# Kernel optimization log

Hardware: AMD Instinct MI355X
Metric: run time of the kernel (lower is better)

Reference implementation:

```python
import jax, jax.numpy as jnp
import numpy as np

H = 128          # hidden_size
IN = 93          # input_size
NL = 4           # num_layers
B, T = 256, 512  # batch, seq_len


def setup_inputs() -> dict:
    key = jax.random.key(0)
    ks = jax.random.split(key, 8)
    s = 1.0 / np.sqrt(H)  # pytorch LSTM init range scale
    x = jax.random.normal(ks[0], (B, T, IN), jnp.float32)
    W_ih0 = jax.random.normal(ks[1], (4 * H, IN), jnp.float32) * s   # layer 0 input weights
    W_ih_rest = jax.random.normal(ks[2], (NL - 1, 4 * H, H), jnp.float32) * s  # layers 1..3
    W_hh = jax.random.normal(ks[3], (NL, 4 * H, H), jnp.float32) * s
    b_ih = jax.random.normal(ks[4], (NL, 4 * H), jnp.float32) * s
    b_hh = jax.random.normal(ks[5], (NL, 4 * H), jnp.float32) * s
    W_fc = jax.random.normal(ks[6], (1, H), jnp.float32) * s
    b_fc = jax.random.normal(ks[7], (1,), jnp.float32) * s
    return {"x": x, "W_ih0": W_ih0, "W_ih_rest": W_ih_rest, "W_hh": W_hh,
            "b_ih": b_ih, "b_hh": b_hh, "W_fc": W_fc, "b_fc": b_fc}


def _lstm_layer(x_tm, W_ih, W_hh_l, bi, bh):
    # x_tm: [T, B, in]; precompute input-side gates as one big GEMM
    gates_x = jnp.einsum('tbi,gi->tbg', x_tm, W_ih) + bi + bh  # [T,B,4H]

    def step(carry, gx):
        h, c = carry
        g = gx + h @ W_hh_l.T                      # [B,4H]
        i, f, gg, o = jnp.split(g, 4, axis=-1)     # pytorch gate order: i,f,g,o
        i = jax.nn.sigmoid(i)
        f = jax.nn.sigmoid(f)
        gg = jnp.tanh(gg)
        o = jax.nn.sigmoid(o)
        c = f * c + i * gg
        h = o * jnp.tanh(c)
        return (h, c), h

    b = x_tm.shape[1]
    h0 = jnp.zeros((b, H), x_tm.dtype)
    (_, _), hs = jax.lax.scan(step, (h0, h0), gates_x)
    return hs  # [T,B,H]


def reference(x, W_ih0, W_ih_rest, W_hh, b_ih, b_hh, W_fc, b_fc):
    # Eval-mode forward (dropout inactive), matching model.eval() semantics.
    h = jnp.transpose(x, (1, 0, 2))  # time-major [T,B,IN]
    h = _lstm_layer(h, W_ih0, W_hh[0], b_ih[0], b_hh[0])
    for l in range(1, NL):
        h = _lstm_layer(h, W_ih_rest[l - 1], W_hh[l], b_ih[l], b_hh[l])
    out = jax.nn.sigmoid(jnp.einsum('tbh,oh->tbo', h, W_fc) + b_fc)  # [T,B,1]
    return jnp.transpose(out, (1, 0, 2))  # [B,T,1]
```

## Files before the change

### kernel.cpp

```cpp
#include <hip/hip_runtime.h>
#include <hip/hip_bf16.h>

#define H_    128
#define IN_   93
#define NL_   4
#define B_    256
#define T_    512
#define G_    512
#define C_    32
#define NCH   (T_ / C_)
#define NLAUNCH (NCH + NL_ - 1)
#define LOG2E 1.44269504088896f
#define BH_   (B_ * H_)
#define B96_  (B_ * 96)

typedef __attribute__((ext_vector_type(8))) short bf16x8;
typedef __attribute__((ext_vector_type(4))) float f32x4;
typedef unsigned long long u64;

#define RCHUNK ((size_t)C_ * BH_)

__device__ __forceinline__ ushort bf16_rn(float f) {
    uint x = __float_as_uint(f);
    uint r = (x + 0x7FFFu + ((x >> 16) & 1u)) >> 16;
    return (ushort)r;
}
__device__ __forceinline__ float exp2_fast(float x) { return __builtin_amdgcn_exp2f(x); }
__device__ __forceinline__ float rcp_fast(float x)  { return __builtin_amdgcn_rcpf(x); }

__global__ void prep_x(const float* __restrict__ x, ushort* __restrict__ xb) {
    int idx = blockIdx.x * 256 + threadIdx.x;
    int t = idx / (B_ * 96);
    int rem = idx % (B_ * 96);
    int b = rem / 96;
    int k = rem % 96;
    float v = 0.0f;
    if (k < IN_) v = x[((size_t)b * T_ + t) * IN_ + k];
    xb[idx] = bf16_rn(v);
}

__global__ void prep_w(const float* __restrict__ Wih0,
                       const float* __restrict__ Wihr,
                       const float* __restrict__ Whh,
                       ushort* __restrict__ Wc) {
    int idx = blockIdx.x * 256 + threadIdx.x;
    int l = idx / (G_ * 256);
    int rem = idx % (G_ * 256);
    int g = rem / 256;
    int k = rem % 256;
    int kx = (l == 0) ? 96 : 128;
    float v = 0.0f;
    if (k < kx) {
        if (l == 0) { if (k < IN_) v = Wih0[g * IN_ + k]; }
        else        { v = Wihr[(((size_t)(l - 1)) * G_ + g) * H_ + k]; }
    } else if (k < kx + H_) {
        v = Whh[(((size_t)l) * G_ + g) * H_ + (k - kx)];
    }
    float scale = (g >= 256 && g < 384) ? (2.0f * LOG2E) : LOG2E;
    Wc[idx] = bf16_rn(v * scale);
}

__global__ void prep_bias(const float* __restrict__ bih,
                          const float* __restrict__ bhh,
                          float* __restrict__ bc) {
    int idx = blockIdx.x * 256 + threadIdx.x;
    int g = idx & 511;
    float scale = (g >= 256 && g < 384) ? (2.0f * LOG2E) : LOG2E;
    bc[idx] = (bih[idx] + bhh[idx]) * scale;
}

#define SWZC(row, col) ((col) ^ (((row) & 7) << 3))
#define XRD(ts, s) (*(const bf16x8*)&hist[(ts) * 2048 + lo * 128 + \
                     ((((s) << 5) | (q << 3)) ^ ((lo & 7) << 3))])
#define HRD(ptr, s) (*(const bf16x8*)&(ptr)[lo * 128 + \
                     ((((s) << 5) | (q << 3)) ^ ((lo & 7) << 3))])
#define MF(a, av, bw) a = __builtin_amdgcn_mfma_f32_16x16x32_bf16(av, bw, a, 0, 0, 0)

__global__ __launch_bounds__(512, 2)
void recur_chunk(const ushort* __restrict__ xb,
                 const ushort* __restrict__ Wc,
                 const float* __restrict__ biasc,
                 ushort* __restrict__ ring,
                 ushort* __restrict__ seed3,
                 float*  __restrict__ cstate,
                 const float* __restrict__ wfc,
                 const float* __restrict__ bfc,
                 float* __restrict__ out,
                 int wlaunch) {
    __shared__ ushort hist[C_ * 16 * 128];
    __shared__ ushort seedb[16 * 128];
    __shared__ float  wfs[H_];

    const int bid = blockIdx.x;
    const int l = bid >> 4;
    const int g = bid & 15;
    const int k = wlaunch - l;
    if (k < 0 || k >= NCH) return;

    const bool lz = (l == 0);
    const int t0 = k * C_;

    const int tid = threadIdx.x;
    const int wv  = tid >> 6;
    const int ln  = tid & 63;
    const int q   = ln >> 4;
    const int lo  = ln & 15;
    const int u   = (wv << 4) | lo;
    const int b0  = g << 4;

    const ushort* Wl = Wc + (size_t)l * G_ * 256;
    const float*  bl = biasc + l * G_;
    const int kx = lz ? 96 : 128;

    ushort* ring_self = ring + (size_t)(2 * l + (k & 1)) * RCHUNK;
    const ushort* ring_up = ring + (size_t)(2 * (l - 1) + (k & 1)) * RCHUNK;

    if (tid < H_) wfs[tid] = wfc[tid];

    for (int i = tid; i < C_ * 16 * 32; i += 512) {
        int t = i >> 9, rem = i & 511, row = rem >> 5, c8 = rem & 31;
        u64 v = 0;
        if (lz) {
            if (c8 < 24)
                v = *(const u64*)(xb + (size_t)(t0 + t) * B96_ +
                                  (size_t)(b0 + row) * 96 + (c8 << 2));
        } else {
            v = *(const u64*)(ring_up + (size_t)t * BH_ +
                              (size_t)(b0 + row) * H_ + (c8 << 2));
        }
        *(u64*)&hist[t * 2048 + row * 128 + SWZC(row, c8 << 2)] = v;
    }

    {
        int row = tid >> 5, c8 = tid & 31;
        u64 v = 0;
        if (k > 0) {
            if (l < 3) {
                v = *(const u64*)(ring + (size_t)(2 * l + ((k - 1) & 1)) * RCHUNK +
                                  (size_t)(C_ - 1) * BH_ +
                                  (size_t)(b0 + row) * H_ + (c8 << 2));
            } else {
                v = *(const u64*)(seed3 + (size_t)(b0 + row) * H_ + (c8 << 2));
            }
        }
        *(u64*)&seedb[row * 128 + SWZC(row, c8 << 2)] = v;
    }

    bf16x8 bwx[4][4], bwh[4][4];
#pragma unroll
    for (int tu = 0; tu < 4; ++tu)
#pragma unroll
        for (int s = 0; s < 4; ++s) {
            const ushort* rowp = Wl + ((size_t)((tu << 7) + u) << 8);
            bwx[tu][s] = *(const bf16x8*)(rowp + (s << 5) + (q << 3));
            bwh[tu][s] = *(const bf16x8*)(rowp + kx + (s << 5) + (q << 3));
        }

    const float bv0 = bl[u];
    const float bv1 = bl[128 + u];
    const float bv2 = bl[256 + u];
    const float bv3 = bl[384 + u];

    f32x4 cc = {0.0f, 0.0f, 0.0f, 0.0f};
    if (k > 0) {
#pragma unroll
        for (int r = 0; r < 4; ++r)
            cc[r] = cstate[(((size_t)(l * 16 + g)) * 16 + (q << 2) + r) * 128 + u];
    }

    __syncthreads();

    f32x4 ac0 = {bv0, bv0, bv0, bv0};
    f32x4 ac1 = {bv1, bv1, bv1, bv1};
    f32x4 ac2 = {bv2, bv2, bv2, bv2};
    f32x4 ac3 = {bv3, bv3, bv3, bv3};
    {
        bf16x8 x0 = XRD(0, 0), x1 = XRD(0, 1), x2 = XRD(0, 2), x3 = XRD(0, 3);
        MF(ac0, x0, bwx[0][0]); MF(ac1, x0, bwx[1][0]); MF(ac2, x0, bwx[2][0]); MF(ac3, x0, bwx[3][0]);
        MF(ac0, x1, bwx[0][1]); MF(ac1, x1, bwx[1][1]); MF(ac2, x1, bwx[2][1]); MF(ac3, x1, bwx[3][1]);
        MF(ac0, x2, bwx[0][2]); MF(ac1, x2, bwx[1][2]); MF(ac2, x2, bwx[2][2]); MF(ac3, x2, bwx[3][2]);
        MF(ac0, x3, bwx[0][3]); MF(ac1, x3, bwx[1][3]); MF(ac2, x3, bwx[2][3]); MF(ac3, x3, bwx[3][3]);
    }

    for (int t = 0; t < C_; ++t) {
        asm volatile("s_waitcnt lgkmcnt(0)" ::: "memory");
        __builtin_amdgcn_s_barrier();
        __builtin_amdgcn_sched_barrier(0);

        const ushort* hsrc = (t == 0) ? seedb : &hist[(t - 1) * 2048];
        bf16x8 h0 = HRD(hsrc, 0), h1 = HRD(hsrc, 1), h2 = HRD(hsrc, 2), h3v = HRD(hsrc, 3);
        MF(ac0, h0, bwh[0][0]); MF(ac1, h0, bwh[1][0]); MF(ac2, h0, bwh[2][0]); MF(ac3, h0, bwh[3][0]);
        MF(ac0, h1, bwh[0][1]); MF(ac1, h1, bwh[1][1]); MF(ac2, h1, bwh[2][1]); MF(ac3, h1, bwh[3][1]);
        MF(ac0, h2, bwh[0][2]); MF(ac1, h2, bwh[1][2]); MF(ac2, h2, bwh[2][2]); MF(ac3, h2, bwh[3][2]);
        MF(ac0, h3v, bwh[0][3]); MF(ac1, h3v, bwh[1][3]); MF(ac2, h3v, bwh[2][3]); MF(ac3, h3v, bwh[3][3]);

        f32x4 an0 = {bv0, bv0, bv0, bv0};
        f32x4 an1 = {bv1, bv1, bv1, bv1};
        f32x4 an2 = {bv2, bv2, bv2, bv2};
        f32x4 an3 = {bv3, bv3, bv3, bv3};
        if (t + 1 < C_) {
            bf16x8 x0 = XRD(t + 1, 0), x1 = XRD(t + 1, 1), x2 = XRD(t + 1, 2), x3 = XRD(t + 1, 3);
            MF(an0, x0, bwx[0][0]); MF(an1, x0, bwx[1][0]); MF(an2, x0, bwx[2][0]); MF(an3, x0, bwx[3][0]);
            MF(an0, x1, bwx[0][1]); MF(an1, x1, bwx[1][1]); MF(an2, x1, bwx[2][1]); MF(an3, x1, bwx[3][1]);
            MF(an0, x2, bwx[0][2]); MF(an1, x2, bwx[1][2]); MF(an2, x2, bwx[2][2]); MF(an3, x2, bwx[3][2]);
            MF(an0, x3, bwx[0][3]); MF(an1, x3, bwx[1][3]); MF(an2, x3, bwx[2][3]); MF(an3, x3, bwx[3][3]);
        }

#pragma unroll
        for (int r = 0; r < 4; ++r) {
            float ei = exp2_fast(fminf(-ac0[r], 60.0f));
            float ef = exp2_fast(-ac1[r]);
            float eg = exp2_fast(fminf(-ac2[r], 60.0f));
            float eo = exp2_fast(fminf(-ac3[r], 60.0f));
            float rf  = rcp_fast(1.0f + ef);
            float rig = rcp_fast((1.0f + ei) * (1.0f + eg));
            float cn  = __builtin_fmaf(cc[r], rf, (1.0f - eg) * rig);
            cc[r] = cn;
            float ec  = exp2_fast(fminf(-2.88539008177793f * cn, 60.0f));
            float roc = rcp_fast((1.0f + eo) * (1.0f + ec));
            float h_  = (1.0f - ec) * roc;
            int row = (q << 2) + r;
            hist[t * 2048 + row * 128 + SWZC(row, u)] = bf16_rn(h_);
        }

        ac0 = an0; ac1 = an1; ac2 = an2; ac3 = an3;
    }

    asm volatile("s_waitcnt lgkmcnt(0)" ::: "memory");
    __builtin_amdgcn_s_barrier();
    __builtin_amdgcn_sched_barrier(0);

    if (l < 3) {
        for (int i = tid; i < C_ * 16 * 32; i += 512) {
            int t = i >> 9, rem = i & 511, row = rem >> 5, c8 = rem & 31;
            u64 v = *(const u64*)&hist[t * 2048 + row * 128 + SWZC(row, c8 << 2)];
            *(u64*)(ring_self + (size_t)t * BH_ +
                    (size_t)(b0 + row) * H_ + (c8 << 2)) = v;
        }
    } else {
        int t = tid >> 4, row = tid & 15;
        float acc = 0.0f;
#pragma unroll 8
        for (int c8 = 0; c8 < 32; ++c8) {
            u64 v = *(const u64*)&hist[t * 2048 + row * 128 + SWZC(row, c8 << 2)];
#pragma unroll
            for (int j = 0; j < 4; ++j) {
                float hvf = __uint_as_float(((uint)(ushort)(v >> (16 * j))) << 16);
                acc = __builtin_fmaf(hvf, wfs[(c8 << 2) + j], acc);
            }
        }
        float z = acc + bfc[0];
        out[(size_t)(b0 + row) * T_ + (t0 + t)] =
            rcp_fast(1.0f + exp2_fast(-z * LOG2E));
        int row2 = tid >> 5, c82 = tid & 31;
        u64 v2 = *(const u64*)&hist[(C_ - 1) * 2048 + row2 * 128 + SWZC(row2, c82 << 2)];
        *(u64*)(seed3 + (size_t)(b0 + row2) * H_ + (c82 << 2)) = v2;
    }

#pragma unroll
    for (int r = 0; r < 4; ++r)
        cstate[(((size_t)(l * 16 + g)) * 16 + (q << 2) + r) * 128 + u] = cc[r];
}

extern "C" void kernel_launch(void* const* d_in, const int* in_sizes, int n_in,
                              void* d_out, int out_size, void* d_ws, size_t ws_size,
                              hipStream_t stream) {
    const float* x    = (const float*)d_in[0];
    const float* Wih0 = (const float*)d_in[1];
    const float* Wihr = (const float*)d_in[2];
    const float* Whh  = (const float*)d_in[3];
    const float* bih  = (const float*)d_in[4];
    const float* bhh  = (const float*)d_in[5];
    const float* Wfc  = (const float*)d_in[6];
    const float* bfc  = (const float*)d_in[7];
    float* out = (float*)d_out;

    char* ws = (char*)d_ws;
    const size_t xb_bytes    = (size_t)T_ * B_ * 96 * 2;
    const size_t wc_bytes    = (size_t)NL_ * G_ * 256 * 2;
    const size_t bias_bytes  = (size_t)NL_ * G_ * 4;
    const size_t ring_bytes  = (size_t)6 * RCHUNK * 2;
    const size_t seed3_bytes = (size_t)B_ * H_ * 2;

    ushort* xb    = (ushort*)ws;
    ushort* Wc    = (ushort*)(ws + xb_bytes);
    float*  biasc = (float*)(ws + xb_bytes + wc_bytes);
    ushort* ring  = (ushort*)(ws + xb_bytes + wc_bytes + bias_bytes);
    ushort* seed3 = (ushort*)(ws + xb_bytes + wc_bytes + bias_bytes + ring_bytes);
    float*  cstate= (float*)(ws + xb_bytes + wc_bytes + bias_bytes + ring_bytes + seed3_bytes);

    prep_x<<<(T_ * B_ * 96) / 256, 256, 0, stream>>>(x, xb);
    prep_w<<<(NL_ * G_ * 256) / 256, 256, 0, stream>>>(Wih0, Wihr, Whh, Wc);
    prep_bias<<<(NL_ * G_) / 256, 256, 0, stream>>>(bih, bhh, biasc);

    for (int w = 0; w < NLAUNCH; ++w) {
        recur_chunk<<<NL_ * 16, 512, 0, stream>>>(xb, Wc, biasc, ring, seed3,
                                                  cstate, Wfc, bfc, out, w);
    }
}
```

Measured before the change: 998.7 us.

## Replace per-wavefront kernel launches with a persistent kernel using flag-based layer pipelining

The 19 sequential wavefront launches become a single persistent kernel in which each layer/batch-group block loops over all time chunks. Blocks wait on their upstream layer through global progress and consumer flags spun on with acquire loads, and the double-buffered ring is guarded by consumer acknowledgements. This keeps weights in registers and the cell state on chip across chunks, removing launch gaps and the cstate and seed reloads. It also widens the LDS swizzle to 16 rows and drops some fminf clamps. The cost is the risk of deadlock if the 64 blocks are not all co-resident, plus spin-polling overhead.

```diff
diff --git a/kernel.cpp b/kernel.cpp
--- a/kernel.cpp
+++ b/kernel.cpp
@@ -9,7 +9,6 @@
 #define G_    512
 #define C_    32
 #define NCH   (T_ / C_)
-#define NLAUNCH (NCH + NL_ - 1)
 #define LOG2E 1.44269504088896f
 #define BH_   (B_ * H_)
 #define B96_  (B_ * 96)
@@ -27,6 +26,14 @@
 }
 __device__ __forceinline__ float exp2_fast(float x) { return __builtin_amdgcn_exp2f(x); }
 __device__ __forceinline__ float rcp_fast(float x)  { return __builtin_amdgcn_rcpf(x); }
+
+__device__ __forceinline__ void spin_acq(int* p, int target) {
+    int v = __hip_atomic_load(p, __ATOMIC_ACQUIRE, __HIP_MEMORY_SCOPE_AGENT);
+    while (v < target) {
+        __builtin_amdgcn_s_sleep(2);
+        v = __hip_atomic_load(p, __ATOMIC_ACQUIRE, __HIP_MEMORY_SCOPE_AGENT);
+    }
+}
 
 __global__ void prep_x(const float* __restrict__ x, ushort* __restrict__ xb) {
     int idx = blockIdx.x * 256 + threadIdx.x;
@@ -69,24 +76,26 @@
     bc[idx] = (bih[idx] + bhh[idx]) * scale;
 }
 
-#define SWZC(row, col) ((col) ^ (((row) & 7) << 3))
+__global__ void zero_flags(int* __restrict__ fl) {
+    if (threadIdx.x < 128) fl[threadIdx.x] = 0;
+}
+
+#define SWZ16(row, col) ((col) ^ (((row) & 15) << 3))
 #define XRD(ts, s) (*(const bf16x8*)&hist[(ts) * 2048 + lo * 128 + \
-                     ((((s) << 5) | (q << 3)) ^ ((lo & 7) << 3))])
+                     ((((s) << 5) | (q << 3)) ^ (lo << 3))])
 #define HRD(ptr, s) (*(const bf16x8*)&(ptr)[lo * 128 + \
-                     ((((s) << 5) | (q << 3)) ^ ((lo & 7) << 3))])
+                     ((((s) << 5) | (q << 3)) ^ (lo << 3))])
 #define MF(a, av, bw) a = __builtin_amdgcn_mfma_f32_16x16x32_bf16(av, bw, a, 0, 0, 0)
 
-__global__ __launch_bounds__(512, 2)
-void recur_chunk(const ushort* __restrict__ xb,
-                 const ushort* __restrict__ Wc,
-                 const float* __restrict__ biasc,
-                 ushort* __restrict__ ring,
-                 ushort* __restrict__ seed3,
-                 float*  __restrict__ cstate,
-                 const float* __restrict__ wfc,
-                 const float* __restrict__ bfc,
-                 float* __restrict__ out,
-                 int wlaunch) {
+__global__ __launch_bounds__(512, 1)
+void recur_persist(const ushort* __restrict__ xb,
+                   const ushort* __restrict__ Wc,
+                   const float* __restrict__ biasc,
+                   ushort* __restrict__ ring,
+                   int*    __restrict__ flags,
+                   const float* __restrict__ wfc,
+                   const float* __restrict__ bfc,
+                   float* __restrict__ out) {
     __shared__ ushort hist[C_ * 16 * 128];
     __shared__ ushort seedb[16 * 128];
     __shared__ float  wfs[H_];
@@ -94,11 +103,7 @@
     const int bid = blockIdx.x;
     const int l = bid >> 4;
     const int g = bid & 15;
-    const int k = wlaunch - l;
-    if (k < 0 || k >= NCH) return;
-
     const bool lz = (l == 0);
-    const int t0 = k * C_;
 
     const int tid = threadIdx.x;
     const int wv  = tid >> 6;
@@ -112,39 +117,16 @@
     const float*  bl = biasc + l * G_;
     const int kx = lz ? 96 : 128;
 
-    ushort* ring_self = ring + (size_t)(2 * l + (k & 1)) * RCHUNK;
-    const ushort* ring_up = ring + (size_t)(2 * (l - 1) + (k & 1)) * RCHUNK;
+    int* prog = flags;
+    int* cons = flags + 64;
+    int* pself = prog + (l * 16 + g);
+    int* pup   = prog + ((l - 1) * 16 + g);
+    int* cself = cons + (l * 16 + g);
+    int* cdown = cons + ((l + 1) * 16 + g);
 
     if (tid < H_) wfs[tid] = wfc[tid];
-
-    for (int i = tid; i < C_ * 16 * 32; i += 512) {
-        int t = i >> 9, rem = i & 511, row = rem >> 5, c8 = rem & 31;
-        u64 v = 0;
-        if (lz) {
-            if (c8 < 24)
-                v = *(const u64*)(xb + (size_t)(t0 + t) * B96_ +
-                                  (size_t)(b0 + row) * 96 + (c8 << 2));
-        } else {
-            v = *(const u64*)(ring_up + (size_t)t * BH_ +
-                              (size_t)(b0 + row) * H_ + (c8 << 2));
-        }
-        *(u64*)&hist[t * 2048 + row * 128 + SWZC(row, c8 << 2)] = v;
-    }
-
-    {
-        int row = tid >> 5, c8 = tid & 31;
-        u64 v = 0;
-        if (k > 0) {
-            if (l < 3) {
-                v = *(const u64*)(ring + (size_t)(2 * l + ((k - 1) & 1)) * RCHUNK +
-                                  (size_t)(C_ - 1) * BH_ +
-                                  (size_t)(b0 + row) * H_ + (c8 << 2));
-            } else {
-                v = *(const u64*)(seed3 + (size_t)(b0 + row) * H_ + (c8 << 2));
-            }
-        }
-        *(u64*)&seedb[row * 128 + SWZC(row, c8 << 2)] = v;
-    }
+    ((u64*)seedb)[tid] = 0ull;
+    const float bfc0 = bfc[0];
 
     bf16x8 bwx[4][4], bwh[4][4];
 #pragma unroll
@@ -155,111 +137,132 @@
             bwx[tu][s] = *(const bf16x8*)(rowp + (s << 5) + (q << 3));
             bwh[tu][s] = *(const bf16x8*)(rowp + kx + (s << 5) + (q << 3));
         }
-
     const float bv0 = bl[u];
     const float bv1 = bl[128 + u];
     const float bv2 = bl[256 + u];
     const float bv3 = bl[384 + u];
 
     f32x4 cc = {0.0f, 0.0f, 0.0f, 0.0f};
-    if (k > 0) {
+
+    for (int k = 0; k < NCH; ++k) {
+        const int t0 = k * C_;
+        ushort* ring_self = ring + (size_t)(2 * l + (k & 1)) * RCHUNK;
+        const ushort* ring_up = ring + (size_t)(2 * (l - 1) + (k & 1)) * RCHUNK;
+
+        if (l > 0) spin_acq(pup, k + 1);
+
+        for (int i = tid; i < C_ * 16 * 32; i += 512) {
+            int t = i >> 9, rem = i & 511, row = rem >> 5, c8 = rem & 31;
+            u64 v = 0;
+            if (lz) {
+                if (c8 < 24)
+                    v = *(const u64*)(xb + (size_t)(t0 + t) * B96_ +
+                                      (size_t)(b0 + row) * 96 + (c8 << 2));
+            } else {
+                v = *(const u64*)(ring_up + (size_t)t * BH_ +
+                                  (size_t)(b0 + row) * H_ + (c8 << 2));
+            }
+            *(u64*)&hist[t * 2048 + row * 128 + SWZ16(row, c8 << 2)] = v;
+        }
+        __syncthreads();
+        if (tid == 0 && l > 0)
+            __hip_atomic_store(cself, k + 1, __ATOMIC_RELAXED, __HIP_MEMORY_SCOPE_AGENT);
+
+        f32x4 ac0 = {bv0, bv0, bv0, bv0};
+        f32x4 ac1 = {bv1, bv1, bv1, bv1};
+        f32x4 ac2 = {bv2, bv2, bv2, bv2};
+        f32x4 ac3 = {bv3, bv3, bv3, bv3};
+        {
+            bf16x8 x0 = XRD(0, 0), x1 = XRD(0, 1), x2 = XRD(0, 2), x3 = XRD(0, 3);
+            MF(ac0, x0, bwx[0][0]); MF(ac1, x0, bwx[1][0]); MF(ac2, x0, bwx[2][0]); MF(ac3, x0, bwx[3][0]);
+            MF(ac0, x1, bwx[0][1]); MF(ac1, x1, bwx[1][1]); MF(ac2, x1, bwx[2][1]); MF(ac3, x1, bwx[3][1]);
+            MF(ac0, x2, bwx[0][2]); MF(ac1, x2, bwx[1][2]); MF(ac2, x2, bwx[2][2]); MF(ac3, x2, bwx[3][2]);
+            MF(ac0, x3, bwx[0][3]); MF(ac1, x3, bwx[1][3]); MF(ac2, x3, bwx[2][3]); MF(ac3, x3, bwx[3][3]);
+        }
+
+        for (int t = 0; t < C_; ++t) {
+            asm volatile("s_waitcnt lgkmcnt(0)" ::: "memory");
+            __builtin_amdgcn_s_barrier();
+            __builtin_amdgcn_sched_barrier(0);
+
+            const ushort* hsrc = (t == 0) ? seedb : &hist[(t - 1) * 2048];
+            bf16x8 h0 = HRD(hsrc, 0), h1 = HRD(hsrc, 1), h2 = HRD(hsrc, 2), h3v = HRD(hsrc, 3);
+            MF(ac0, h0, bwh[0][0]); MF(ac1, h0, bwh[1][0]); MF(ac2, h0, bwh[2][0]); MF(ac3, h0, bwh[3][0]);
+            MF(ac0, h1, bwh[0][1]); MF(ac1, h1, bwh[1][1]); MF(ac2, h1, bwh[2][1]); MF(ac3, h1, bwh[3][1]);
+            MF(ac0, h2, bwh[0][2]); MF(ac1, h2, bwh[1][2]); MF(ac2, h2, bwh[2][2]); MF(ac3, h2, bwh[3][2]);
+            MF(ac0, h3v, bwh[0][3]); MF(ac1, h3v, bwh[1][3]); MF(ac2, h3v, bwh[2][3]); MF(ac3, h3v, bwh[3][3]);
+
+            f32x4 an0 = {bv0, bv0, bv0, bv0};
+            f32x4 an1 = {bv1, bv1, bv1, bv1};
+            f32x4 an2 = {bv2, bv2, bv2, bv2};
+            f32x4 an3 = {bv3, bv3, bv3, bv3};
+            if (t + 1 < C_) {
+                bf16x8 x0 = XRD(t + 1, 0), x1 = XRD(t + 1, 1), x2 = XRD(t + 1, 2), x3 = XRD(t + 1, 3);
+                MF(an0, x0, bwx[0][0]); MF(an1, x0, bwx[1][0]); MF(an2, x0, bwx[2][0]); MF(an3, x0, bwx[3][0]);
+                MF(an0, x1, bwx[0][1]); MF(an1, x1, bwx[1][1]); MF(an2, x1, bwx[2][1]); MF(an3, x1, bwx[3][1]);
+                MF(an0, x2, bwx[0][2]); MF(an1, x2, bwx[1][2]); MF(an2, x2, bwx[2][2]); MF(an3, x2, bwx[3][2]);
+                MF(an0, x3, bwx[0][3]); MF(an1, x3, bwx[1][3]); MF(an2, x3, bwx[2][3]); MF(an3, x3, bwx[3][3]);
+            }
+
 #pragma unroll
-        for (int r = 0; r < 4; ++r)
-            cc[r] = cstate[(((size_t)(l * 16 + g)) * 16 + (q << 2) + r) * 128 + u];
-    }
-
-    __syncthreads();
-
-    f32x4 ac0 = {bv0, bv0, bv0, bv0};
-    f32x4 ac1 = {bv1, bv1, bv1, bv1};
-    f32x4 ac2 = {bv2, bv2, bv2, bv2};
-    f32x4 ac3 = {bv3, bv3, bv3, bv3};
-    {
-        bf16x8 x0 = XRD(0, 0), x1 = XRD(0, 1), x2 = XRD(0, 2), x3 = XRD(0, 3);
-        MF(ac0, x0, bwx[0][0]); MF(ac1, x0, bwx[1][0]); MF(ac2, x0, bwx[2][0]); MF(ac3, x0, bwx[3][0]);
-        MF(ac0, x1, bwx[0][1]); MF(ac1, x1, bwx[1][1]); MF(ac2, x1, bwx[2][1]); MF(ac3, x1, bwx[3][1]);
-        MF(ac0, x2, bwx[0][2]); MF(ac1, x2, bwx[1][2]); MF(ac2, x2, bwx[2][2]); MF(ac3, x2, bwx[3][2]);
-        MF(ac0, x3, bwx[0][3]); MF(ac1, x3, bwx[1][3]); MF(ac2, x3, bwx[2][3]); MF(ac3, x3, bwx[3][3]);
-    }
-
-    for (int t = 0; t < C_; ++t) {
+            for (int r = 0; r < 4; ++r) {
+                float ei = exp2_fast(-ac0[r]);
+                float ef = exp2_fast(-ac1[r]);
+                float eg = exp2_fast(fminf(-ac2[r], 60.0f));
+                float eo = exp2_fast(-ac3[r]);
+                float rf  = rcp_fast(1.0f + ef);
+                float rig = rcp_fast((1.0f + ei) * (1.0f + eg));
+                float cn  = __builtin_fmaf(cc[r], rf, (1.0f - eg) * rig);
+                cc[r] = cn;
+                float ec  = exp2_fast(fminf(-2.88539008177793f * cn, 60.0f));
+                float roc = rcp_fast((1.0f + eo) * (1.0f + ec));
+                float h_  = (1.0f - ec) * roc;
+                int row = (q << 2) + r;
+                hist[t * 2048 + row * 128 + SWZ16(row, u)] = bf16_rn(h_);
+            }
+            ac0 = an0; ac1 = an1; ac2 = an2; ac3 = an3;
+        }
+
         asm volatile("s_waitcnt lgkmcnt(0)" ::: "memory");
         __builtin_amdgcn_s_barrier();
         __builtin_amdgcn_sched_barrier(0);
 
-        const ushort* hsrc = (t == 0) ? seedb : &hist[(t - 1) * 2048];
-        bf16x8 h0 = HRD(hsrc, 0), h1 = HRD(hsrc, 1), h2 = HRD(hsrc, 2), h3v = HRD(hsrc, 3);
-        MF(ac0, h0, bwh[0][0]); MF(ac1, h0, bwh[1][0]); MF(ac2, h0, bwh[2][0]); MF(ac3, h0, bwh[3][0]);
-        MF(ac0, h1, bwh[0][1]); MF(ac1, h1, bwh[1][1]); MF(ac2, h1, bwh[2][1]); MF(ac3, h1, bwh[3][1]);
-        MF(ac0, h2, bwh[0][2]); MF(ac1, h2, bwh[1][2]); MF(ac2, h2, bwh[2][2]); MF(ac3, h2, bwh[3][2]);
-        MF(ac0, h3v, bwh[0][3]); MF(ac1, h3v, bwh[1][3]); MF(ac2, h3v, bwh[2][3]); MF(ac3, h3v, bwh[3][3]);
-
-        f32x4 an0 = {bv0, bv0, bv0, bv0};
-        f32x4 an1 = {bv1, bv1, bv1, bv1};
-        f32x4 an2 = {bv2, bv2, bv2, bv2};
-        f32x4 an3 = {bv3, bv3, bv3, bv3};
-        if (t + 1 < C_) {
-            bf16x8 x0 = XRD(t + 1, 0), x1 = XRD(t + 1, 1), x2 = XRD(t + 1, 2), x3 = XRD(t + 1, 3);
-            MF(an0, x0, bwx[0][0]); MF(an1, x0, bwx[1][0]); MF(an2, x0, bwx[2][0]); MF(an3, x0, bwx[3][0]);
-            MF(an0, x1, bwx[0][1]); MF(an1, x1, bwx[1][1]); MF(an2, x1, bwx[2][1]); MF(an3, x1, bwx[3][1]);
-            MF(an0, x2, bwx[0][2]); MF(an1, x2, bwx[1][2]); MF(an2, x2, bwx[2][2]); MF(an3, x2, bwx[3][2]);
-            MF(an0, x3, bwx[0][3]); MF(an1, x3, bwx[1][3]); MF(an2, x3, bwx[2][3]); MF(an3, x3, bwx[3][3]);
-        }
-
+        {
+            int row = tid >> 5, c8 = tid & 31;
+            u64 v = *(const u64*)&hist[(C_ - 1) * 2048 + row * 128 + SWZ16(row, c8 << 2)];
+            *(u64*)&seedb[row * 128 + SWZ16(row, c8 << 2)] = v;
+        }
+
+        if (l < 3 && k >= 2) spin_acq(cdown, k - 1);
+
+        if (l < 3) {
+            for (int i = tid; i < C_ * 16 * 32; i += 512) {
+                int t = i >> 9, rem = i & 511, row = rem >> 5, c8 = rem & 31;
+                u64 v = *(const u64*)&hist[t * 2048 + row * 128 + SWZ16(row, c8 << 2)];
+                *(u64*)(ring_self + (size_t)t * BH_ +
+                        (size_t)(b0 + row) * H_ + (c8 << 2)) = v;
+            }
+        } else {
+            int t = tid >> 4, row = tid & 15;
+            float acc = 0.0f;
+#pragma unroll 8
+            for (int c8 = 0; c8 < 32; ++c8) {
+                u64 v = *(const u64*)&hist[t * 2048 + row * 128 + SWZ16(row, c8 << 2)];
 #pragma unroll
-        for (int r = 0; r < 4; ++r) {
-            float ei = exp2_fast(fminf(-ac0[r], 60.0f));
-            float ef = exp2_fast(-ac1[r]);
-            float eg = exp2_fast(fminf(-ac2[r], 60.0f));
-            float eo = exp2_fast(fminf(-ac3[r], 60.0f));
-            float rf  = rcp_fast(1.0f + ef);
-            float rig = rcp_fast((1.0f + ei) * (1.0f + eg));
-            float cn  = __builtin_fmaf(cc[r], rf, (1.0f - eg) * rig);
-            cc[r] = cn;
-            float ec  = exp2_fast(fminf(-2.88539008177793f * cn, 60.0f));
-            float roc = rcp_fast((1.0f + eo) * (1.0f + ec));
-            float h_  = (1.0f - ec) * roc;
-            int row = (q << 2) + r;
-            hist[t * 2048 + row * 128 + SWZC(row, u)] = bf16_rn(h_);
-        }
-
-        ac0 = an0; ac1 = an1; ac2 = an2; ac3 = an3;
+                for (int j = 0; j < 4; ++j) {
+                    float hvf = __uint_as_float(((uint)(ushort)(v >> (16 * j))) << 16);
+                    acc = __builtin_fmaf(hvf, wfs[(c8 << 2) + j], acc);
+                }
+            }
+            float z = acc + bfc0;
+            out[(size_t)(b0 + row) * T_ + (t0 + t)] =
+                rcp_fast(1.0f + exp2_fast(-z * LOG2E));
+        }
+
+        __syncthreads();
+        if (tid == 0 && l < 3)
+            __hip_atomic_store(pself, k + 1, __ATOMIC_RELEASE, __HIP_MEMORY_SCOPE_AGENT);
     }
-
-    asm volatile("s_waitcnt lgkmcnt(0)" ::: "memory");
-    __builtin_amdgcn_s_barrier();
-    __builtin_amdgcn_sched_barrier(0);
-
-    if (l < 3) {
-        for (int i = tid; i < C_ * 16 * 32; i += 512) {
-            int t = i >> 9, rem = i & 511, row = rem >> 5, c8 = rem & 31;
-            u64 v = *(const u64*)&hist[t * 2048 + row * 128 + SWZC(row, c8 << 2)];
-            *(u64*)(ring_self + (size_t)t * BH_ +
-                    (size_t)(b0 + row) * H_ + (c8 << 2)) = v;
-        }
-    } else {
-        int t = tid >> 4, row = tid & 15;
-        float acc = 0.0f;
-#pragma unroll 8
-        for (int c8 = 0; c8 < 32; ++c8) {
-            u64 v = *(const u64*)&hist[t * 2048 + row * 128 + SWZC(row, c8 << 2)];
-#pragma unroll
-            for (int j = 0; j < 4; ++j) {
-                float hvf = __uint_as_float(((uint)(ushort)(v >> (16 * j))) << 16);
-                acc = __builtin_fmaf(hvf, wfs[(c8 << 2) + j], acc);
-            }
-        }
-        float z = acc + bfc[0];
-        out[(size_t)(b0 + row) * T_ + (t0 + t)] =
-            rcp_fast(1.0f + exp2_fast(-z * LOG2E));
-        int row2 = tid >> 5, c82 = tid & 31;
-        u64 v2 = *(const u64*)&hist[(C_ - 1) * 2048 + row2 * 128 + SWZC(row2, c82 << 2)];
-        *(u64*)(seed3 + (size_t)(b0 + row2) * H_ + (c82 << 2)) = v2;
-    }
-
-#pragma unroll
-    for (int r = 0; r < 4; ++r)
-        cstate[(((size_t)(l * 16 + g)) * 16 + (q << 2) + r) * 128 + u] = cc[r];
 }
 
 extern "C" void kernel_launch(void* const* d_in, const int* in_sizes, int n_in,
@@ -280,21 +283,20 @@
     const size_t wc_bytes    = (size_t)NL_ * G_ * 256 * 2;
     const size_t bias_bytes  = (size_t)NL_ * G_ * 4;
     const size_t ring_bytes  = (size_t)6 * RCHUNK * 2;
-    const size_t seed3_bytes = (size_t)B_ * H_ * 2;
+    const size_t flag_bytes  = 128 * 4;
 
     ushort* xb    = (ushort*)ws;
     ushort* Wc    = (ushort*)(ws + xb_bytes);
     float*  biasc = (float*)(ws + xb_bytes + wc_bytes);
     ushort* ring  = (ushort*)(ws + xb_bytes + wc_bytes + bias_bytes);
-    ushort* seed3 = (ushort*)(ws + xb_bytes + wc_bytes + bias_bytes + ring_bytes);
-    float*  cstate= (float*)(ws + xb_bytes + wc_bytes + bias_bytes + ring_bytes + seed3_bytes);
+    int*    flags = (int*)(ws + xb_bytes + wc_bytes + bias_bytes + ring_bytes);
+    (void)flag_bytes;
 
     prep_x<<<(T_ * B_ * 96) / 256, 256, 0, stream>>>(x, xb);
     prep_w<<<(NL_ * G_ * 256) / 256, 256, 0, stream>>>(Wih0, Wihr, Whh, Wc);
     prep_bias<<<(NL_ * G_) / 256, 256, 0, stream>>>(bih, bhh, biasc);
-
-    for (int w = 0; w < NLAUNCH; ++w) {
-        recur_chunk<<<NL_ * 16, 512, 0, stream>>>(xb, Wc, biasc, ring, seed3,
-                                                  cstate, Wfc, bfc, out, w);
-    }
-}
+    zero_flags<<<1, 256, 0, stream>>>(flags);
+
+    recur_persist<<<NL_ * 16, 512, 0, stream>>>(xb, Wc, biasc, ring, flags,
+                                                Wfc, bfc, out);
+}
```

Result: faster. 887.4 us, median of 2 (-11.1%).
